# Performance work log

Hardware: AMD Instinct MI355X
Metric: run time of the kernel (lower is better)

## Reference

```python
import jax, jax.numpy as jnp
import numpy as np

N_HEADS = 16
DIM = 1024
HEAD_DIM = DIM // N_HEADS

def setup_inputs() -> dict:
    key = jax.random.key(0)
    ks = jax.random.split(key, 5)
    B, S = 4, 2048
    x = jax.random.normal(ks[0], (B, S, DIM), dtype=jnp.float32)
    # PyTorch Linear-style params (stored as [in, out] for x @ W)
    sc = 1.0 / np.sqrt(DIM)
    W_qkv = jax.random.uniform(ks[1], (DIM, 3 * DIM), jnp.float32, -sc, sc)
    b_qkv = jax.random.uniform(ks[2], (3 * DIM,), jnp.float32, -sc, sc)
    W_o = jax.random.uniform(ks[3], (DIM, DIM), jnp.float32, -sc, sc)
    b_o = jax.random.uniform(ks[4], (DIM,), jnp.float32, -sc, sc)
    return {"x": x, "W_qkv": W_qkv, "b_qkv": b_qkv, "W_o": W_o, "b_o": b_o}

def reference(x, W_qkv, b_qkv, W_o, b_o):
    B, S, D = x.shape
    qkv = x @ W_qkv + b_qkv                       # [B,S,3D]
    q, k, v = jnp.split(qkv, 3, axis=2)
    # [B,S,D] -> [B,H,S,hd]
    q = q.reshape(B, S, N_HEADS, HEAD_DIM).transpose(0, 2, 1, 3)
    k = k.reshape(B, S, N_HEADS, HEAD_DIM).transpose(0, 2, 1, 3)
    v = v.reshape(B, S, N_HEADS, HEAD_DIM).transpose(0, 2, 1, 3)
    aff = jnp.einsum('bhqd,bhkd->bhqk', q, k) / jnp.sqrt(jnp.float32(HEAD_DIM))
    causal = jnp.tril(jnp.ones((S, S), dtype=bool))  # [S,S]
    aff = jnp.where(causal[None, None], aff, jnp.float32(-jnp.inf))
    attn = jax.nn.softmax(aff, axis=3)
    # dropout p=0.0 (eval): identity
    out = jnp.einsum('bhqk,bhkd->bhqd', attn, v)
    out = out.transpose(0, 2, 1, 3).reshape(B, S, D)
    return out @ W_o + b_o
```

## Files before the change

### kernel.cpp

```cpp
#include <hip/hip_runtime.h>

typedef unsigned short u16;
typedef short bf16x8 __attribute__((ext_vector_type(8)));
typedef float f32x4 __attribute__((ext_vector_type(4)));
typedef unsigned short ushort8v __attribute__((ext_vector_type(8)));
typedef unsigned short us4 __attribute__((ext_vector_type(4)));
typedef float f4v __attribute__((ext_vector_type(4)));

#define LOG2E 1.4426950408889634f
#define FIXMAX_C (12.0f * LOG2E)

static __device__ __forceinline__ float bf2f(u16 h) {
    unsigned int u = ((unsigned int)h) << 16;
    return __builtin_bit_cast(float, u);
}
static __device__ __forceinline__ u16 f2bf(float f) {
    unsigned int u = __builtin_bit_cast(unsigned int, f);
    u += 0x7FFFu + ((u >> 16) & 1u);
    return (u16)(u >> 16);
}
static __device__ __forceinline__ void ld_lds16(const u16* g, u16* l) {
    __builtin_amdgcn_global_load_lds((const __attribute__((address_space(1))) void*)g,
                                     (__attribute__((address_space(3))) void*)l, 16, 0, 0);
}
#define MFMA16(a, b, c) __builtin_amdgcn_mfma_f32_16x16x32_bf16(a, b, c, 0, 0, 0)
#define SW(r, g) (((r) << 6) + ((((g) ^ ((r) & 7))) << 3))

__global__ void cvt_cast(const float* __restrict__ src, u16* __restrict__ dst, int n4) {
    int i = blockIdx.x * blockDim.x + threadIdx.x;
    const int stride = gridDim.x * blockDim.x;
    for (; i < n4; i += stride) {
        f4v v = *(const f4v*)(src + (size_t)i * 4);
        us4 o;
        o[0] = f2bf(v[0]); o[1] = f2bf(v[1]); o[2] = f2bf(v[2]); o[3] = f2bf(v[3]);
        *(us4*)(dst + (size_t)i * 4) = o;
    }
}

__global__ __launch_bounds__(256) void cvt_T(const float* __restrict__ W, u16* __restrict__ WT,
                                             int N, int K) {
    __shared__ u16 tT[64][72];
    const int tid = threadIdx.x;
    const int tiles_n = N >> 6;
    const int tn = blockIdx.x % tiles_n, tk = blockIdx.x / tiles_n;
    const int rr = tid >> 4, c4 = (tid & 15) * 4;
    #pragma unroll
    for (int i = 0; i < 4; i++) {
        int kk = rr + i * 16;
        f4v v = *(const f4v*)&W[(size_t)(tk * 64 + kk) * N + tn * 64 + c4];
        #pragma unroll
        for (int j = 0; j < 4; j++) tT[c4 + j][kk] = f2bf(v[j]);
    }
    __syncthreads();
    const int nrow = tid >> 2, kc = (tid & 3) * 16;
    ushort8v a = *(const ushort8v*)&tT[nrow][kc];
    ushort8v b = *(const ushort8v*)&tT[nrow][kc + 8];
    u16* dst = WT + (size_t)(tn * 64 + nrow) * K + tk * 64 + kc;
    *(ushort8v*)dst = a;
    *(ushort8v*)(dst + 8) = b;
}

template <int MODE>
__global__ __launch_bounds__(256) void gemm128(
        const u16* __restrict__ A, const u16* __restrict__ BT,
        const u16* __restrict__ bias, void* __restrict__ Cout,
        u16* __restrict__ vT, int K, int nx) {
    __shared__ u16 As[2][128][32];
    __shared__ u16 Bs[2][128][32];
    const int tid = threadIdx.x, lane = tid & 63, wid = tid >> 6;
    const int lm = lane & 15, q = lane >> 4;
    const int id = blockIdx.x;
    const int panel = id / (nx * 8), rem = id % (nx * 8);
    const int bx = rem >> 3, by = panel * 8 + (rem & 7);
    const int m0 = by * 128, n0 = bx * 128;
    const int wm = (wid >> 1) * 64, wn = (wid & 1) * 64;
    const int w32 = wid * 32;
    f32x4 acc[4][4] = {};

    const u16* gA = A + (size_t)(m0 + w32 + (lane >> 2)) * K + (lane & 3) * 8;
    const u16* gB = BT + (size_t)(n0 + w32 + (lane >> 2)) * K + (lane & 3) * 8;

    for (int kb = 0; kb < K; kb += 64) {
        __syncthreads();
        #pragma unroll
        for (int h = 0; h < 2; h++)
            #pragma unroll
            for (int i = 0; i < 2; i++) {
                ld_lds16(gA + kb + h * 32 + (size_t)i * 16 * K, &As[h][w32 + i * 16][0]);
                ld_lds16(gB + kb + h * 32 + (size_t)i * 16 * K, &Bs[h][w32 + i * 16][0]);
            }
        __syncthreads();
        #pragma unroll
        for (int kk = 0; kk < 2; kk++) {
            bf16x8 af[4], bfr[4];
            #pragma unroll
            for (int mi = 0; mi < 4; mi++) af[mi] = *(const bf16x8*)&As[kk][wm + mi * 16 + lm][q * 8];
            #pragma unroll
            for (int ni = 0; ni < 4; ni++) bfr[ni] = *(const bf16x8*)&Bs[kk][wn + ni * 16 + lm][q * 8];
            #pragma unroll
            for (int mi = 0; mi < 4; mi++)
                #pragma unroll
                for (int ni = 0; ni < 4; ni++)
                    acc[mi][ni] = MFMA16(af[mi], bfr[ni], acc[mi][ni]);
        }
    }

    if constexpr (MODE == 0) {
        u16* qkout = (u16*)Cout;
        if (n0 < 2048) {
            #pragma unroll
            for (int ni = 0; ni < 4; ni++) {
                int col = n0 + wn + ni * 16 + lm;
                float bsv = bf2f(bias[col]);
                float sc = (col < 1024) ? 0.125f : 1.0f;
                #pragma unroll
                for (int mi = 0; mi < 4; mi++)
                    #pragma unroll
                    for (int r = 0; r < 4; r++) {
                        int row = m0 + wm + mi * 16 + q * 4 + r;
                        qkout[(size_t)row * 2048 + col] = f2bf((acc[mi][ni][r] + bsv) * sc);
                    }
            }
        } else {
            const int b_ = m0 >> 11;
            const int sb = (m0 & 2047) + wm;
            #pragma unroll
            for (int ni = 0; ni < 4; ni++) {
                int col = n0 + wn + ni * 16 + lm;
                int hh = (col - 2048) >> 6, dd = (col - 2048) & 63;
                float bsv = bf2f(bias[col]);
                u16* dst = vT + ((size_t)((b_ * 16 + hh) * 64 + dd)) * 2048;
                #pragma unroll
                for (int mi = 0; mi < 4; mi++) {
                    us4 pk;
                    #pragma unroll
                    for (int r = 0; r < 4; r++) pk[r] = f2bf(acc[mi][ni][r] + bsv);
                    *(us4*)&dst[sb + mi * 16 + q * 4] = pk;
                }
            }
        }
    } else {
        float* out = (float*)Cout;
        #pragma unroll
        for (int ni = 0; ni < 4; ni++) {
            int col = n0 + wn + ni * 16 + lm;
            float bsv = bf2f(bias[col]);
            #pragma unroll
            for (int mi = 0; mi < 4; mi++)
                #pragma unroll
                for (int r = 0; r < 4; r++) {
                    int row = m0 + wm + mi * 16 + q * 4 + r;
                    out[(size_t)row * 1024 + col] = acc[mi][ni][r] + bsv;
                }
        }
    }
}

template <bool DIAG>
__device__ __forceinline__ void proc_tile(
        const bf16x8* qf, const u16* __restrict__ ksv, const u16* __restrict__ vsv,
        u16* __restrict__ psw, f32x4* o, f32x4& lacc, const bf16x8 ones,
        int lm, int q, int m0w) {
    f32x4 s[4] = {};
    __builtin_amdgcn_s_setprio(1);
    #pragma unroll
    for (int g2 = 0; g2 < 2; g2++) {
        bf16x8 a = qf[g2];
        #pragma unroll
        for (int nt = 0; nt < 4; nt++) {
            bf16x8 bb = *(const bf16x8*)&ksv[SW(nt * 16 + lm, q + 4 * g2)];
            s[nt] = MFMA16(a, bb, s[nt]);
        }
    }
    __builtin_amdgcn_s_setprio(0);
    #pragma unroll
    for (int nt = 0; nt < 4; nt++)
        #pragma unroll
        for (int r = 0; r < 4; r++) {
            float v = s[nt][r];
            if constexpr (DIAG) {
                if (nt * 16 + lm > m0w + q * 4 + r) v = -3e30f;
            }
            float pv = __builtin_amdgcn_exp2f(v * LOG2E - FIXMAX_C);
            psw[SW(q * 4 + r, 2 * nt + (lm >> 3)) + (lm & 7)] = f2bf(pv);
        }
    __builtin_amdgcn_s_setprio(1);
    #pragma unroll
    for (int g2 = 0; g2 < 2; g2++) {
        bf16x8 ap = *(const bf16x8*)&psw[SW(lm, q + 4 * g2)];
        lacc = MFMA16(ap, ones, lacc);
        #pragma unroll
        for (int nt = 0; nt < 4; nt++) {
            bf16x8 bv = *(const bf16x8*)&vsv[SW(nt * 16 + lm, q + 4 * g2)];
            o[nt] = MFMA16(ap, bv, o[nt]);
        }
    }
    __builtin_amdgcn_s_setprio(0);
}

__global__ __launch_bounds__(256, 2) void attn3(
        const u16* __restrict__ qk, const u16* __restrict__ vT, u16* __restrict__ aw) {
    __shared__ u16 smem[16384];
    u16* ks = smem;
    u16* vs = smem + 4096;
    const int tid = threadIdx.x, lane = tid & 63, wid = tid >> 6;
    const int lm = lane & 15, q = lane >> 4;
    const int bh = blockIdx.x, p = blockIdx.y;
    const int b = bh >> 4, h = bh & 15;
    const int t[4] = {p, 15 - p, 16 + p, 31 - p};
    const size_t rowbase = (size_t)b * 2048;
    const int lr = tid >> 2, lcg = (tid & 3) * 2, lc = (tid & 3) * 16;
    const int m0w = wid * 16;
    u16* psw = smem + 8192 + wid * 1024;

    bf16x8 ones;
    #pragma unroll
    for (int j = 0; j < 8; j++) ones[j] = (short)0x3F80;

    #pragma unroll
    for (int i = 0; i < 4; i++) {
        const u16* qa = qk + (rowbase + t[i] * 64 + lr) * 2048 + h * 64 + lc;
        *(ushort8v*)&smem[i * 4096 + SW(lr, lcg)]     = *(const ushort8v*)qa;
        *(ushort8v*)&smem[i * 4096 + SW(lr, lcg + 1)] = *(const ushort8v*)(qa + 8);
    }
    __syncthreads();
    bf16x8 qf[4][2];
    #pragma unroll
    for (int i = 0; i < 4; i++)
        #pragma unroll
        for (int g2 = 0; g2 < 2; g2++)
            qf[i][g2] = *(const bf16x8*)&smem[i * 4096 + SW(m0w + lm, q + 4 * g2)];

    f32x4 o[4][4] = {};
    f32x4 lacc[4] = {};

    const u16* kg = qk + (rowbase + lr) * 2048 + 1024 + h * 64 + lc;
    const u16* vg = vT + ((size_t)bh * 64 + lr) * 2048 + lc;
    const int jmax = t[3];

    ushort8v k0 = *(const ushort8v*)kg, k1 = *(const ushort8v*)(kg + 8);
    ushort8v v0 = *(const ushort8v*)vg, v1 = *(const ushort8v*)(vg + 8);

    for (int jt = 0; jt <= jmax; ++jt) {
        __syncthreads();
        *(ushort8v*)&ks[SW(lr, lcg)] = k0; *(ushort8v*)&ks[SW(lr, lcg + 1)] = k1;
        *(ushort8v*)&vs[SW(lr, lcg)] = v0; *(ushort8v*)&vs[SW(lr, lcg + 1)] = v1;
        __syncthreads();
        if (jt < jmax) {
            const u16* kgj = kg + (size_t)(jt + 1) * 64 * 2048;
            const u16* vgj = vg + (jt + 1) * 64;
            k0 = *(const ushort8v*)kgj; k1 = *(const ushort8v*)(kgj + 8);
            v0 = *(const ushort8v*)vgj; v1 = *(const ushort8v*)(vgj + 8);
        }
        #pragma unroll
        for (int i = 0; i < 4; i++) {
            if (jt < t[i])
                proc_tile<false>(qf[i], ks, vs, psw, o[i], lacc[i], ones, lm, q, m0w);
            else if (jt == t[i])
                proc_tile<true>(qf[i], ks, vs, psw, o[i], lacc[i], ones, lm, q, m0w);
        }
    }

    #pragma unroll
    for (int i = 0; i < 4; i++) {
        f32x4 li;
        #pragma unroll
        for (int r = 0; r < 4; r++) li[r] = __builtin_amdgcn_rcpf(lacc[i][r]);
        #pragma unroll
        for (int nt = 0; nt < 4; nt++)
            #pragma unroll
            for (int r = 0; r < 4; r++) {
                int row = t[i] * 64 + m0w + q * 4 + r;
                int col = h * 64 + nt * 16 + lm;
                aw[(rowbase + row) * 1024 + col] = f2bf(o[i][nt][r] * li[r]);
            }
    }
}

extern "C" void kernel_launch(void* const* d_in, const int* in_sizes, int n_in,
                              void* d_out, int out_size, void* d_ws, size_t ws_size,
                              hipStream_t stream) {
    const float* x    = (const float*)d_in[0];
    const float* Wqkv = (const float*)d_in[1];
    const float* bqkv = (const float*)d_in[2];
    const float* Wo   = (const float*)d_in[3];
    const float* bo   = (const float*)d_in[4];
    float* out = (float*)d_out;

    u16* xb     = (u16*)d_ws;
    u16* WqkvT  = xb + (size_t)8192 * 1024;
    u16* bqkvb  = WqkvT + (size_t)3072 * 1024;
    u16* WoT    = bqkvb + 3072;
    u16* bob    = WoT + (size_t)1024 * 1024;
    u16* qk     = bob + 1024;
    u16* vT     = qk + (size_t)8192 * 2048;
    u16* aw     = vT + (size_t)64 * 64 * 2048;

    cvt_cast<<<2048, 256, 0, stream>>>(x, xb, 8192 * 1024 / 4);
    cvt_cast<<<3,    256, 0, stream>>>(bqkv, bqkvb, 3072 / 4);
    cvt_cast<<<1,    256, 0, stream>>>(bo, bob, 1024 / 4);
    cvt_T<<<48 * 16, 256, 0, stream>>>(Wqkv, WqkvT, 3072, 1024);
    cvt_T<<<16 * 16, 256, 0, stream>>>(Wo, WoT, 1024, 1024);

    gemm128<0><<<24 * 64, 256, 0, stream>>>(xb, WqkvT, bqkvb, qk, vT, 1024, 24);
    attn3<<<dim3(64, 8), 256, 0, stream>>>(qk, vT, aw);
    gemm128<1><<<8 * 64, 256, 0, stream>>>(aw, WoT, bob, out, nullptr, 1024, 8);
}
```

Measured before the change: 270.1 us.

## Replace QKV projection GEMM with 256x256 tile, deep-pipelined, swizzled-LDS kernel

The QKV projection now runs in a new 512-thread kernel that computes 256x256 output tiles. Operands stream through 128KB of dynamic LDS via direct global-to-LDS loads, kept several stages ahead using vmcnt waits. LDS reads are XOR-swizzled to avoid bank conflicts, MFMA bursts are wrapped in s_setprio, and blocks are remapped for L2 locality. This should raise arithmetic intensity and hide memory latency in the largest GEMM, at the cost of one block per CU, fewer blocks (384) and hand-tuned barrier and waitcnt correctness risk.

Measured after the change: 279.1 us. 1.03x slower.

```diff
diff --git a/kernel.cpp b/kernel.cpp
--- a/kernel.cpp
+++ b/kernel.cpp
@@ -58,6 +58,127 @@
     u16* dst = WT + (size_t)(tn * 64 + nrow) * K + tk * 64 + kc;
     *(ushort8v*)dst = a;
     *(ushort8v*)(dst + 8) = b;
+}
+
+static __device__ __forceinline__ void stage_half256(
+        u16* sm, const u16* __restrict__ A, const u16* __restrict__ BT,
+        int m0, int n0, int s, int wid, int lane, int sw_src) {
+    const int ts = s >> 2, h = s & 3, ab = h & 1, kk = h >> 1, buf = ts & 1;
+    const u16* G = (ab ? BT + (size_t)n0 * 1024 : A + (size_t)m0 * 1024)
+                   + (size_t)ts * 64 + kk * 32 + sw_src;
+    u16* L = sm + buf * 32768 + ab * 16384 + kk * 8192 + wid * 1024;
+    const int r0 = wid * 32 + (lane >> 2);
+    ld_lds16(G + (size_t)r0 * 1024,        L);
+    ld_lds16(G + (size_t)(r0 + 16) * 1024, L + 512);
+}
+
+#define AFR(bufc, kkc, mi) (*(const bf16x8*)&sm[(bufc) * 32768 + (kkc) * 8192 + aoff + (mi) * 512])
+#define BFR(bufc, kkc, ni) (*(const bf16x8*)&sm[(bufc) * 32768 + 16384 + (kkc) * 8192 + boff + (ni) * 512])
+
+#define PH(bufc, kkc, nhc, sidx, DOA, VMSTMT) do {                                  \
+    if (DOA) {                                                                      \
+        _Pragma("unroll")                                                           \
+        for (int mi = 0; mi < 8; mi++) af[mi] = AFR(bufc, kkc, mi);                 \
+    }                                                                               \
+    b0 = BFR(bufc, kkc, (nhc) * 2);                                                 \
+    b1 = BFR(bufc, kkc, (nhc) * 2 + 1);                                             \
+    { int s_ = (sidx); if (s_ < 64) stage_half256(sm, A, BT, m0, n0, s_, wid, lane, sw_src); } \
+    asm volatile("" ::: "memory");                                                  \
+    __builtin_amdgcn_s_barrier();                                                   \
+    asm volatile("s_waitcnt lgkmcnt(0)" ::: "memory");                              \
+    __builtin_amdgcn_s_setprio(1);                                                  \
+    _Pragma("unroll")                                                               \
+    for (int mi = 0; mi < 8; mi++) {                                                \
+        acc[mi][(nhc) * 2]     = MFMA16(af[mi], b0, acc[mi][(nhc) * 2]);            \
+        acc[mi][(nhc) * 2 + 1] = MFMA16(af[mi], b1, acc[mi][(nhc) * 2 + 1]);        \
+    }                                                                               \
+    __builtin_amdgcn_s_setprio(0);                                                  \
+    VMSTMT;                                                                         \
+    __builtin_amdgcn_s_barrier();                                                   \
+    asm volatile("" ::: "memory");                                                  \
+} while (0)
+
+__global__ __launch_bounds__(512) void gemm256q(
+        const u16* __restrict__ A, const u16* __restrict__ BT,
+        const u16* __restrict__ bias, u16* __restrict__ qkout, u16* __restrict__ vT) {
+    extern __shared__ u16 sm[];
+    const int tid = threadIdx.x, lane = tid & 63, wid = tid >> 6;
+    const int lm = lane & 15, q = lane >> 4;
+    const int wm_id = wid >> 2, wn_id = wid & 3;
+
+    const int id = blockIdx.x;
+    const int swz = (id & 7) * 48 + (id >> 3);
+    const int by = swz / 12, bx = swz % 12;
+    const int m0 = by * 256, n0 = bx * 256;
+
+    const int swg = (q ^ ((lm >> 1) & 3)) * 8;
+    const int aoff = (wm_id * 128 + lm) * 32 + swg;
+    const int boff = (wn_id * 64 + lm) * 32 + swg;
+    const int sw_src = ((lane & 3) ^ ((lane >> 3) & 3)) * 8;
+
+    f32x4 acc[8][4] = {};
+    bf16x8 af[8], b0, b1;
+
+    #pragma unroll
+    for (int s = 0; s < 7; ++s) stage_half256(sm, A, BT, m0, n0, s, wid, lane, sw_src);
+    asm volatile("s_waitcnt vmcnt(6)" ::: "memory");
+    __builtin_amdgcn_s_barrier();
+
+    #pragma unroll 1
+    for (int i = 0; i < 8; ++i) {
+        const bool deep = (i < 7);
+        {
+            const int t = 2 * i;
+            PH(0, 0, 0, 4 * t + 7, 1, );
+            PH(0, 0, 1, 4 * t + 8, 0, );
+            PH(0, 1, 0, 4 * t + 9, 1, );
+            PH(0, 1, 1, 4 * t + 10, 0,
+               if (deep) asm volatile("s_waitcnt vmcnt(6)" ::: "memory");
+               else      asm volatile("s_waitcnt vmcnt(0)" ::: "memory"));
+        }
+        {
+            const int t = 2 * i + 1;
+            PH(1, 0, 0, 4 * t + 7, 1, );
+            PH(1, 0, 1, 4 * t + 8, 0, );
+            PH(1, 1, 0, 4 * t + 9, 1, );
+            PH(1, 1, 1, 4 * t + 10, 0,
+               if (deep) asm volatile("s_waitcnt vmcnt(6)" ::: "memory");
+               else      asm volatile("s_waitcnt vmcnt(0)" ::: "memory"));
+        }
+    }
+
+    if (n0 < 2048) {
+        #pragma unroll
+        for (int ni = 0; ni < 4; ni++) {
+            int col = n0 + wn_id * 64 + ni * 16 + lm;
+            float bsv = bf2f(bias[col]);
+            float sc = (col < 1024) ? 0.125f : 1.0f;
+            #pragma unroll
+            for (int mi = 0; mi < 8; mi++)
+                #pragma unroll
+                for (int r = 0; r < 4; r++) {
+                    int row = m0 + wm_id * 128 + mi * 16 + q * 4 + r;
+                    qkout[(size_t)row * 2048 + col] = f2bf((acc[mi][ni][r] + bsv) * sc);
+                }
+        }
+    } else {
+        const int b_ = m0 >> 11;
+        const int sb = (m0 & 2047) + wm_id * 128;
+        #pragma unroll
+        for (int ni = 0; ni < 4; ni++) {
+            int col = n0 + wn_id * 64 + ni * 16 + lm;
+            int hh = (col - 2048) >> 6, dd = (col - 2048) & 63;
+            float bsv = bf2f(bias[col]);
+            u16* dst = vT + ((size_t)((b_ * 16 + hh) * 64 + dd)) * 2048;
+            #pragma unroll
+            for (int mi = 0; mi < 8; mi++) {
+                us4 pk;
+                #pragma unroll
+                for (int r = 0; r < 4; r++) pk[r] = f2bf(acc[mi][ni][r] + bsv);
+                *(us4*)&dst[sb + mi * 16 + q * 4] = pk;
+            }
+        }
+    }
 }
 
 template <int MODE>
@@ -106,39 +227,7 @@
     }
 
     if constexpr (MODE == 0) {
-        u16* qkout = (u16*)Cout;
-        if (n0 < 2048) {
-            #pragma unroll
-            for (int ni = 0; ni < 4; ni++) {
-                int col = n0 + wn + ni * 16 + lm;
-                float bsv = bf2f(bias[col]);
-                float sc = (col < 1024) ? 0.125f : 1.0f;
-                #pragma unroll
-                for (int mi = 0; mi < 4; mi++)
-                    #pragma unroll
-                    for (int r = 0; r < 4; r++) {
-                        int row = m0 + wm + mi * 16 + q * 4 + r;
-                        qkout[(size_t)row * 2048 + col] = f2bf((acc[mi][ni][r] + bsv) * sc);
-                    }
-            }
-        } else {
-            const int b_ = m0 >> 11;
-            const int sb = (m0 & 2047) + wm;
-            #pragma unroll
-            for (int ni = 0; ni < 4; ni++) {
-                int col = n0 + wn + ni * 16 + lm;
-                int hh = (col - 2048) >> 6, dd = (col - 2048) & 63;
-                float bsv = bf2f(bias[col]);
-                u16* dst = vT + ((size_t)((b_ * 16 + hh) * 64 + dd)) * 2048;
-                #pragma unroll
-                for (int mi = 0; mi < 4; mi++) {
-                    us4 pk;
-                    #pragma unroll
-                    for (int r = 0; r < 4; r++) pk[r] = f2bf(acc[mi][ni][r] + bsv);
-                    *(us4*)&dst[sb + mi * 16 + q * 4] = pk;
-                }
-            }
-        }
+        (void)vT;
     } else {
         float* out = (float*)Cout;
         #pragma unroll
@@ -296,13 +385,20 @@
     u16* vT     = qk + (size_t)8192 * 2048;
     u16* aw     = vT + (size_t)64 * 64 * 2048;
 
+    static bool attr_done = false;
+    if (!attr_done) {
+        hipFuncSetAttribute(reinterpret_cast<const void*>(gemm256q),
+                            hipFuncAttributeMaxDynamicSharedMemorySize, 131072);
+        attr_done = true;
+    }
+
     cvt_cast<<<2048, 256, 0, stream>>>(x, xb, 8192 * 1024 / 4);
     cvt_cast<<<3,    256, 0, stream>>>(bqkv, bqkvb, 3072 / 4);
     cvt_cast<<<1,    256, 0, stream>>>(bo, bob, 1024 / 4);
     cvt_T<<<48 * 16, 256, 0, stream>>>(Wqkv, WqkvT, 3072, 1024);
     cvt_T<<<16 * 16, 256, 0, stream>>>(Wo, WoT, 1024, 1024);
 
-    gemm128<0><<<24 * 64, 256, 0, stream>>>(xb, WqkvT, bqkvb, qk, vT, 1024, 24);
+    gemm256q<<<384, 512, 131072, stream>>>(xb, WqkvT, bqkvb, qk, vT);
     attn3<<<dim3(64, 8), 256, 0, stream>>>(qk, vT, aw);
     gemm128<1><<<8 * 64, 256, 0, stream>>>(aw, WoT, bob, out, nullptr, 1024, 8);
 }
```

## Replace 128x128 GEMM with 256x128 double-buffered, swizzled, phase-pipelined GEMM

Applied to the files above, without the earlier changes.

Replaces the 128x128 tile GEMM used for the QKV and output projections with a 256x128 tile kernel using 512 threads and 96KB of dynamic LDS. LDS is double-buffered with XOR swizzling to avoid bank conflicts. Next-tile global-to-LDS loads are split across two compute phases and gated by explicit vmcnt waits and barriers, so loads overlap the MFMAs. Block IDs are remapped for L2 locality. The larger tile and LDS footprint lower occupancy, and the hand-tuned waitcnt scheme depends on K being hardcoded to 1024.

Result: no change. 266.0 us (-1.5%).

```diff
diff --git a/kernel.cpp b/kernel.cpp
--- a/kernel.cpp
+++ b/kernel.cpp
@@ -60,48 +60,112 @@
     *(ushort8v*)(dst + 8) = b;
 }
 
-template <int MODE>
-__global__ __launch_bounds__(256) void gemm128(
+#define STG_P0(nb, ts) do {                                      \
+    const u16* ga_ = gA + (ts) * 64;                             \
+    const u16* gb_ = gB + (ts) * 64;                             \
+    u16* la_ = lA + (nb) * 24576;                                \
+    u16* lb_ = lB + (nb) * 24576;                                \
+    ld_lds16(ga_,      la_);                       \
+    ld_lds16(ga_ + 32, la_ + 8192);                \
+    ld_lds16(gb_,      lb_);                       \
+} while (0)
+#define STG_P1(nb, ts) do {                                      \
+    const u16* ga_ = gA + 131072 + (ts) * 64;                    \
+    const u16* gb_ = gB + (ts) * 64;                             \
+    u16* la_ = lA + (nb) * 24576 + 4096;                         \
+    u16* lb_ = lB + (nb) * 24576 + 4096;                         \
+    ld_lds16(gb_ + 32, lb_);                       \
+    ld_lds16(ga_,      la_);                       \
+    ld_lds16(ga_ + 32, la_ + 8192);                \
+} while (0)
+
+#define PHASE(bufc, qd, DOSTG, STG, VMST) do {                                           \
+    bf16x8 paf[4][2]; bf16x8 pbf[2][2];                                                  \
+    _Pragma("unroll")                                                                    \
+    for (int m_ = 0; m_ < 4; m_++) {                                                     \
+        paf[m_][0] = *(const bf16x8*)&sm[(bufc)*24576 + (qd)*4096 + aro + m_*512];       \
+        paf[m_][1] = *(const bf16x8*)&sm[(bufc)*24576 + 8192 + (qd)*4096 + aro + m_*512];\
+    }                                                                                    \
+    _Pragma("unroll")                                                                    \
+    for (int n_ = 0; n_ < 2; n_++) {                                                     \
+        pbf[n_][0] = *(const bf16x8*)&sm[(bufc)*24576 + 16384 + bro + n_*512];           \
+        pbf[n_][1] = *(const bf16x8*)&sm[(bufc)*24576 + 20480 + bro + n_*512];           \
+    }                                                                                    \
+    if (DOSTG) { STG; }                                                                  \
+    asm volatile("" ::: "memory");                                                       \
+    __builtin_amdgcn_s_barrier();                                                        \
+    asm volatile("s_waitcnt lgkmcnt(0)" ::: "memory");                                   \
+    __builtin_amdgcn_sched_barrier(0);                                                   \
+    __builtin_amdgcn_s_setprio(1);                                                       \
+    _Pragma("unroll")                                                                    \
+    for (int m_ = 0; m_ < 4; m_++)                                                       \
+        _Pragma("unroll")                                                                \
+        for (int n_ = 0; n_ < 2; n_++) {                                                 \
+            acc[(qd)*4+m_][n_] = MFMA16(paf[m_][0], pbf[n_][0], acc[(qd)*4+m_][n_]);     \
+            acc[(qd)*4+m_][n_] = MFMA16(paf[m_][1], pbf[n_][1], acc[(qd)*4+m_][n_]);     \
+        }                                                                                \
+    __builtin_amdgcn_s_setprio(0);                                                       \
+    VMST;                                                                                \
+    __builtin_amdgcn_s_barrier();                                                        \
+    asm volatile("" ::: "memory");                                                       \
+} while (0)
+
+template <int MODE, int NBX>
+__global__ __launch_bounds__(512) void gemm256(
         const u16* __restrict__ A, const u16* __restrict__ BT,
         const u16* __restrict__ bias, void* __restrict__ Cout,
-        u16* __restrict__ vT, int K, int nx) {
-    __shared__ u16 As[2][128][32];
-    __shared__ u16 Bs[2][128][32];
+        u16* __restrict__ vT) {
+    extern __shared__ u16 sm[];
     const int tid = threadIdx.x, lane = tid & 63, wid = tid >> 6;
     const int lm = lane & 15, q = lane >> 4;
+    const int wm_id = wid >> 2, wn_id = wid & 3;
+
     const int id = blockIdx.x;
-    const int panel = id / (nx * 8), rem = id % (nx * 8);
-    const int bx = rem >> 3, by = panel * 8 + (rem & 7);
-    const int m0 = by * 128, n0 = bx * 128;
-    const int wm = (wid >> 1) * 64, wn = (wid & 1) * 64;
-    const int w32 = wid * 32;
-    f32x4 acc[4][4] = {};
-
-    const u16* gA = A + (size_t)(m0 + w32 + (lane >> 2)) * K + (lane & 3) * 8;
-    const u16* gB = BT + (size_t)(n0 + w32 + (lane >> 2)) * K + (lane & 3) * 8;
-
-    for (int kb = 0; kb < K; kb += 64) {
-        __syncthreads();
-        #pragma unroll
-        for (int h = 0; h < 2; h++)
-            #pragma unroll
-            for (int i = 0; i < 2; i++) {
-                ld_lds16(gA + kb + h * 32 + (size_t)i * 16 * K, &As[h][w32 + i * 16][0]);
-                ld_lds16(gB + kb + h * 32 + (size_t)i * 16 * K, &Bs[h][w32 + i * 16][0]);
-            }
-        __syncthreads();
-        #pragma unroll
-        for (int kk = 0; kk < 2; kk++) {
-            bf16x8 af[4], bfr[4];
-            #pragma unroll
-            for (int mi = 0; mi < 4; mi++) af[mi] = *(const bf16x8*)&As[kk][wm + mi * 16 + lm][q * 8];
-            #pragma unroll
-            for (int ni = 0; ni < 4; ni++) bfr[ni] = *(const bf16x8*)&Bs[kk][wn + ni * 16 + lm][q * 8];
-            #pragma unroll
-            for (int mi = 0; mi < 4; mi++)
-                #pragma unroll
-                for (int ni = 0; ni < 4; ni++)
-                    acc[mi][ni] = MFMA16(af[mi], bfr[ni], acc[mi][ni]);
+    const int swz = (id & 7) * (NBX * 4) + (id >> 3);
+    const int by = swz / NBX, bx = swz % NBX;
+    const int m0 = by * 256, n0 = bx * 128;
+
+    const int sw = (q ^ ((lm >> 1) & 3)) * 8;
+    const int aro = (wm_id * 64 + lm) * 32 + sw;
+    const int bro = (wn_id * 32 + lm) * 32 + sw;
+
+    const int sw_src = ((lane & 3) ^ ((lane >> 3) & 3)) * 8;
+    const int srow = wid * 16 + (lane >> 2);
+    const u16* gA = A + (size_t)(m0 + srow) * 1024 + sw_src;
+    const u16* gB = BT + (size_t)(n0 + srow) * 1024 + sw_src;
+    u16* lA = sm + wid * 512;
+    u16* lB = sm + 16384 + wid * 512;
+
+    f32x4 acc[8][2] = {};
+
+    ld_lds16(gA, lA);
+    ld_lds16(gA + 32, lA + 8192);
+    ld_lds16(gB, lB);
+    ld_lds16(gB + 32, lB + 4096);
+    ld_lds16(gA + 131072, lA + 4096);
+    ld_lds16(gA + 131072 + 32, lA + 8192 + 4096);
+    asm volatile("s_waitcnt vmcnt(2)" ::: "memory");
+    __builtin_amdgcn_s_barrier();
+
+    #pragma unroll 1
+    for (int i = 0; i < 8; ++i) {
+        {
+            const int t = 2 * i, ts1 = t + 1;
+            const bool dostg = (ts1 < 16);
+            PHASE(0, 0, dostg, STG_P0(1, ts1),
+                  if (t < 15) asm volatile("s_waitcnt vmcnt(3)" ::: "memory");
+                  else        asm volatile("s_waitcnt vmcnt(0)" ::: "memory"));
+            PHASE(0, 1, dostg, STG_P1(1, ts1),
+                  if (t < 15) asm volatile("s_waitcnt vmcnt(2)" ::: "memory"));
+        }
+        {
+            const int t = 2 * i + 1, ts1 = t + 1;
+            const bool dostg = (ts1 < 16);
+            PHASE(1, 0, dostg, STG_P0(0, ts1),
+                  if (t < 15) asm volatile("s_waitcnt vmcnt(3)" ::: "memory");
+                  else        asm volatile("s_waitcnt vmcnt(0)" ::: "memory"));
+            PHASE(1, 1, dostg, STG_P1(0, ts1),
+                  if (t < 15) asm volatile("s_waitcnt vmcnt(2)" ::: "memory"));
         }
     }
 
@@ -109,49 +173,50 @@
         u16* qkout = (u16*)Cout;
         if (n0 < 2048) {
             #pragma unroll
-            for (int ni = 0; ni < 4; ni++) {
-                int col = n0 + wn + ni * 16 + lm;
+            for (int ni = 0; ni < 2; ni++) {
+                int col = n0 + wn_id * 32 + ni * 16 + lm;
                 float bsv = bf2f(bias[col]);
                 float sc = (col < 1024) ? 0.125f : 1.0f;
                 #pragma unroll
-                for (int mi = 0; mi < 4; mi++)
+                for (int mi = 0; mi < 8; mi++) {
+                    int rowb = m0 + (mi >> 2) * 128 + wm_id * 64 + (mi & 3) * 16 + q * 4;
                     #pragma unroll
-                    for (int r = 0; r < 4; r++) {
-                        int row = m0 + wm + mi * 16 + q * 4 + r;
-                        qkout[(size_t)row * 2048 + col] = f2bf((acc[mi][ni][r] + bsv) * sc);
-                    }
+                    for (int r = 0; r < 4; r++)
+                        qkout[(size_t)(rowb + r) * 2048 + col] = f2bf((acc[mi][ni][r] + bsv) * sc);
+                }
             }
         } else {
             const int b_ = m0 >> 11;
-            const int sb = (m0 & 2047) + wm;
+            const int sbb = (m0 & 2047);
             #pragma unroll
-            for (int ni = 0; ni < 4; ni++) {
-                int col = n0 + wn + ni * 16 + lm;
+            for (int ni = 0; ni < 2; ni++) {
+                int col = n0 + wn_id * 32 + ni * 16 + lm;
                 int hh = (col - 2048) >> 6, dd = (col - 2048) & 63;
                 float bsv = bf2f(bias[col]);
                 u16* dst = vT + ((size_t)((b_ * 16 + hh) * 64 + dd)) * 2048;
                 #pragma unroll
-                for (int mi = 0; mi < 4; mi++) {
+                for (int mi = 0; mi < 8; mi++) {
+                    int rw = sbb + (mi >> 2) * 128 + wm_id * 64 + (mi & 3) * 16 + q * 4;
                     us4 pk;
                     #pragma unroll
                     for (int r = 0; r < 4; r++) pk[r] = f2bf(acc[mi][ni][r] + bsv);
-                    *(us4*)&dst[sb + mi * 16 + q * 4] = pk;
+                    *(us4*)&dst[rw] = pk;
                 }
             }
         }
     } else {
         float* out = (float*)Cout;
         #pragma unroll
-        for (int ni = 0; ni < 4; ni++) {
-            int col = n0 + wn + ni * 16 + lm;
+        for (int ni = 0; ni < 2; ni++) {
+            int col = n0 + wn_id * 32 + ni * 16 + lm;
             float bsv = bf2f(bias[col]);
             #pragma unroll
-            for (int mi = 0; mi < 4; mi++)
+            for (int mi = 0; mi < 8; mi++) {
+                int rowb = m0 + (mi >> 2) * 128 + wm_id * 64 + (mi & 3) * 16 + q * 4;
                 #pragma unroll
-                for (int r = 0; r < 4; r++) {
-                    int row = m0 + wm + mi * 16 + q * 4 + r;
-                    out[(size_t)row * 1024 + col] = acc[mi][ni][r] + bsv;
-                }
+                for (int r = 0; r < 4; r++)
+                    out[(size_t)(rowb + r) * 1024 + col] = acc[mi][ni][r] + bsv;
+            }
         }
     }
 }
@@ -296,13 +361,22 @@
     u16* vT     = qk + (size_t)8192 * 2048;
     u16* aw     = vT + (size_t)64 * 64 * 2048;
 
+    static bool attr_done = false;
+    if (!attr_done) {
+        hipFuncSetAttribute(reinterpret_cast<const void*>(gemm256<0, 24>),
+                            hipFuncAttributeMaxDynamicSharedMemorySize, 98304);
+        hipFuncSetAttribute(reinterpret_cast<const void*>(gemm256<1, 8>),
+                            hipFuncAttributeMaxDynamicSharedMemorySize, 98304);
+        attr_done = true;
+    }
+
     cvt_cast<<<2048, 256, 0, stream>>>(x, xb, 8192 * 1024 / 4);
     cvt_cast<<<3,    256, 0, stream>>>(bqkv, bqkvb, 3072 / 4);
     cvt_cast<<<1,    256, 0, stream>>>(bo, bob, 1024 / 4);
     cvt_T<<<48 * 16, 256, 0, stream>>>(Wqkv, WqkvT, 3072, 1024);
     cvt_T<<<16 * 16, 256, 0, stream>>>(Wo, WoT, 1024, 1024);
 
-    gemm128<0><<<24 * 64, 256, 0, stream>>>(xb, WqkvT, bqkvb, qk, vT, 1024, 24);
+    gemm256<0, 24><<<768, 512, 98304, stream>>>(xb, WqkvT, bqkvb, qk, vT);
     attn3<<<dim3(64, 8), 256, 0, stream>>>(qk, vT, aw);
-    gemm128<1><<<8 * 64, 256, 0, stream>>>(aw, WoT, bob, out, nullptr, 1024, 8);
-}
+    gemm256<1, 8><<<256, 512, 98304, stream>>>(aw, WoT, bob, out, nullptr);
+}
```
